# Kernel tuning notes

Hardware: AMD Instinct MI355X
Metric: run time of the kernel (lower is better)

Reference implementation:

```python
import jax, jax.numpy as jnp
import numpy as np

LEN_C = 1024
LR = 0.01
GAMMA = 0.999
R, S, E = 4, 4, 4


def setup_inputs() -> dict:
    key = jax.random.key(0)
    k1, k2, k3 = jax.random.split(key, 3)
    Fx = jax.random.normal(k1, (R, S, E, LEN_C), dtype=jnp.float32)
    Dis = jax.random.normal(k2, (E, LEN_C), dtype=jnp.float32)
    initial_weights = jax.random.normal(k3, (R, S, LEN_C), dtype=jnp.float32) * 0.02
    return {"Fx": Fx, "Dis": Dis, "initial_weights": initial_weights}


def reference(Fx, Dis, initial_weights):
    len_c = Fx.shape[-1]
    # --- first_grad: one-step adaptation gradient (detached in original torch code) ---
    w0 = jax.lax.stop_gradient(initial_weights)
    anti = jnp.einsum('rsen,rsn->e', Fx, w0)           # [E]
    error = Dis[:, -1] - anti                           # [E]
    # d/dw of sum_e error_e^2 with error = Dis - Fx.w  =>  -2 * Fx^T error
    weights_grad = jax.lax.stop_gradient(-2.0 * jnp.einsum('rsen,e->rsn', Fx, error))
    control_weights = initial_weights - 0.5 * LR * weights_grad  # [R,S,N]
    # --- build_delay_line, vectorized Toeplitz gather:
    # Fx_extend[t, r, s, e, n] = Fx[r, s, e, t-n] if t >= n else 0
    t = jnp.arange(len_c)
    idx = t[:, None] - t[None, :]                       # [T, N]
    mask = idx >= 0
    safe_idx = jnp.where(mask, idx, 0)
    Fx_ext = jnp.where(mask, Fx[..., safe_idx], jnp.float32(0.0))  # [R,S,E,T,N]
    # --- adaptive_filtering: sum over r, s, n ---
    anti_noise_matrix = jnp.einsum('rsetn,rsn->te', Fx_ext, control_weights)  # [T,E]
    gamma_vector = jnp.power(jnp.float32(GAMMA), (len_c - 1 - t).astype(jnp.float32))
    return anti_noise_matrix, gamma_vector
```

## Files before the change

### kernel.cpp

```cpp
#include <hip/hip_runtime.h>

#define LEN_C 1024
#define LR_F 0.01f
#define GAMMA_F 0.999f

__global__ __launch_bounds__(256) void k_fused(const float* __restrict__ Fx,
                                               const float* __restrict__ Dis,
                                               const float* __restrict__ w0,
                                               float* __restrict__ out) {
    int bid = blockIdx.x;
    int tid = threadIdx.x;
    int e = bid / 40;
    int r = bid % 40;
    int Tb, Nb;
    if (r < 4)       { Tb = 0; Nb = r; }
    else if (r < 12) { Tb = 1; Nb = r - 4; }
    else if (r < 24) { Tb = 2; Nb = r - 12; }
    else             { Tb = 3; Nb = r - 24; }
    const int T0 = Tb * 256, N0 = Nb * 64;
    const int B = T0 - N0 - 63;

    __shared__ __align__(16) float sFx[16 * 320];
    __shared__ __align__(16) float sCw[16 * 64];
    __shared__ float sPart[4][4];
    __shared__ float sErr[4];

    if (bid < 4) {
        int g = bid * 256 + tid;
        out[4 * LEN_C + g] = powf(GAMMA_F, (float)(LEN_C - 1 - g));
    }

    for (int rs = 0; rs < 16; ++rs) {
        const float* src = Fx + (rs * 4 + e) * LEN_C;
        for (int m = tid; m < 320; m += 256) {
            int k = B + m;
            sFx[rs * 320 + m] = ((unsigned)k < (unsigned)LEN_C) ? src[k] : 0.f;
        }
    }

    float a0 = 0.f, a1 = 0.f, a2 = 0.f, a3 = 0.f;
    #pragma unroll 4
    for (int i = tid; i < 4096; i += 256) {
        int rs = i >> 8;
        int n4 = i & 255;
        const float4* fx = (const float4*)(Fx + rs * (4 * LEN_C)) + n4;
        float4 wv = ((const float4*)(w0 + rs * LEN_C))[n4];
        float4 f0 = fx[0], f1 = fx[256], f2 = fx[512], f3 = fx[768];
        a0 += f0.x * wv.x + f0.y * wv.y + f0.z * wv.z + f0.w * wv.w;
        a1 += f1.x * wv.x + f1.y * wv.y + f1.z * wv.z + f1.w * wv.w;
        a2 += f2.x * wv.x + f2.y * wv.y + f2.z * wv.z + f2.w * wv.w;
        a3 += f3.x * wv.x + f3.y * wv.y + f3.z * wv.z + f3.w * wv.w;
    }
    for (int off = 32; off > 0; off >>= 1) {
        a0 += __shfl_down(a0, off, 64);
        a1 += __shfl_down(a1, off, 64);
        a2 += __shfl_down(a2, off, 64);
        a3 += __shfl_down(a3, off, 64);
    }
    int w = tid >> 6, l = tid & 63;
    if (l == 0) { sPart[w][0] = a0; sPart[w][1] = a1; sPart[w][2] = a2; sPart[w][3] = a3; }
    __syncthreads();
    if (tid < 4) {
        float anti = sPart[0][tid] + sPart[1][tid] + sPart[2][tid] + sPart[3][tid];
        sErr[tid] = Dis[tid * LEN_C + (LEN_C - 1)] - anti;
    }
    __syncthreads();

    {
        int rs = tid >> 4, j4 = (tid & 15) * 4;
        int n = N0 + j4;
        const float* base = Fx + rs * (4 * LEN_C) + n;
        float4 wv = *(const float4*)(w0 + rs * LEN_C + n);
        float4 f0 = *(const float4*)(base);
        float4 f1 = *(const float4*)(base + LEN_C);
        float4 f2 = *(const float4*)(base + 2 * LEN_C);
        float4 f3 = *(const float4*)(base + 3 * LEN_C);
        float e0 = sErr[0], e1 = sErr[1], e2 = sErr[2], e3 = sErr[3];
        float4 c;
        c.x = wv.x + LR_F * (f0.x * e0 + f1.x * e1 + f2.x * e2 + f3.x * e3);
        c.y = wv.y + LR_F * (f0.y * e0 + f1.y * e1 + f2.y * e2 + f3.y * e3);
        c.z = wv.z + LR_F * (f0.z * e0 + f1.z * e1 + f2.z * e2 + f3.z * e3);
        c.w = wv.w + LR_F * (f0.w * e0 + f1.w * e1 + f2.w * e2 + f3.w * e3);
        *(float4*)(sCw + rs * 64 + j4) = c;
    }
    __syncthreads();

    int i0 = l * 4;
    float acc0 = 0.f, acc1 = 0.f, acc2 = 0.f, acc3 = 0.f;
    #pragma unroll
    for (int rr = 0; rr < 4; ++rr) {
        int rs = w * 4 + rr;
        const float* crow = sCw + rs * 64;
        const float* frow = sFx + rs * 320;
        int M = i0 + 60;
        float4 flo = *(const float4*)(frow + M);
        float4 fhi = *(const float4*)(frow + M + 4);
        #pragma unroll
        for (int jb = 0; jb < 16; ++jb) {
            float4 c = *(const float4*)(crow + jb * 4);
            float v0 = flo.x, v1 = flo.y, v2 = flo.z, v3 = flo.w;
            float v4 = fhi.x, v5 = fhi.y, v6 = fhi.z;
            acc0 += v3 * c.x + v2 * c.y + v1 * c.z + v0 * c.w;
            acc1 += v4 * c.x + v3 * c.y + v2 * c.z + v1 * c.w;
            acc2 += v5 * c.x + v4 * c.y + v3 * c.z + v2 * c.w;
            acc3 += v6 * c.x + v5 * c.y + v4 * c.z + v3 * c.w;
            fhi = flo;
            M -= 4;
            if (jb < 15) flo = *(const float4*)(frow + M);
        }
    }

    __syncthreads();
    float* sred = sFx;
    sred[w * 256 + i0 + 0] = acc0;
    sred[w * 256 + i0 + 1] = acc1;
    sred[w * 256 + i0 + 2] = acc2;
    sred[w * 256 + i0 + 3] = acc3;
    __syncthreads();
    float sum = sred[tid] + sred[256 + tid] + sred[512 + tid] + sred[768 + tid];
    atomicAdd(&out[(T0 + tid) * 4 + e], sum);
}

extern "C" void kernel_launch(void* const* d_in, const int* in_sizes, int n_in,
                              void* d_out, int out_size, void* d_ws, size_t ws_size,
                              hipStream_t stream) {
    const float* Fx  = (const float*)d_in[0];
    const float* Dis = (const float*)d_in[1];
    const float* w0  = (const float*)d_in[2];
    float* out = (float*)d_out;

    hipMemsetAsync(d_out, 0, 4 * LEN_C * sizeof(float), stream);
    k_fused<<<160, 256, 0, stream>>>(Fx, Dis, w0, out);
}
```

Measured before the change: 73.66 us.

## Give each block a 32-row output tile over the full causal range, drop memset and atomics

Work is re-partitioned so each of 128 blocks owns 32 consecutive output rows for one channel and covers that row range's whole causal triangle. Each wave splits the reduction across 8 lane groups and combines them with shuffles, then writes the result directly. This removes the separate memset launch and the global atomics. In exchange the blocks are unevenly loaded, each needs about 136 KB of shared memory, and every block recomputes the full control weights for its range.

```diff
diff --git a/kernel.cpp b/kernel.cpp
--- a/kernel.cpp
+++ b/kernel.cpp
@@ -4,37 +4,38 @@
 #define LR_F 0.01f
 #define GAMMA_F 0.999f
 
-__global__ __launch_bounds__(256) void k_fused(const float* __restrict__ Fx,
-                                               const float* __restrict__ Dis,
-                                               const float* __restrict__ w0,
-                                               float* __restrict__ out) {
-    int bid = blockIdx.x;
-    int tid = threadIdx.x;
-    int e = bid / 40;
-    int r = bid % 40;
-    int Tb, Nb;
-    if (r < 4)       { Tb = 0; Nb = r; }
-    else if (r < 12) { Tb = 1; Nb = r - 4; }
-    else if (r < 24) { Tb = 2; Nb = r - 12; }
-    else             { Tb = 3; Nb = r - 24; }
-    const int T0 = Tb * 256, N0 = Nb * 64;
-    const int B = T0 - N0 - 63;
+__global__ __launch_bounds__(256) void k_one(const float* __restrict__ Fx,
+                                             const float* __restrict__ Dis,
+                                             const float* __restrict__ w0,
+                                             float* __restrict__ out) {
+    const int bid = blockIdx.x;
+    const int tid = threadIdx.x;
+    const int e  = bid >> 5;
+    const int Tb = bid & 31;
+    const int T0 = Tb << 5;
+    const int P  = T0 + 32;
+    const int S  = P >> 3;
 
-    __shared__ __align__(16) float sFx[16 * 320];
-    __shared__ __align__(16) float sCw[16 * 64];
+    __shared__ __align__(16) float sFx[16 * 1120];
+    __shared__ __align__(16) float sCw[16 * 1024];
+    __shared__ float sRed[128];
     __shared__ float sPart[4][4];
     __shared__ float sErr[4];
 
     if (bid < 4) {
-        int g = bid * 256 + tid;
+        int g = (bid << 8) + tid;
         out[4 * LEN_C + g] = powf(GAMMA_F, (float)(LEN_C - 1 - g));
     }
 
+    const int W = P + 64;
     for (int rs = 0; rs < 16; ++rs) {
         const float* src = Fx + (rs * 4 + e) * LEN_C;
-        for (int m = tid; m < 320; m += 256) {
-            int k = B + m;
-            sFx[rs * 320 + m] = ((unsigned)k < (unsigned)LEN_C) ? src[k] : 0.f;
+        float* dst = sFx + rs * 1120;
+        for (int m = tid; m < W; m += 256) {
+            int k = m - 63;
+            float v = 0.f;
+            if ((unsigned)k < (unsigned)LEN_C) v = src[k];
+            dst[m] = v;
         }
     }
 
@@ -57,7 +58,7 @@
         a2 += __shfl_down(a2, off, 64);
         a3 += __shfl_down(a3, off, 64);
     }
-    int w = tid >> 6, l = tid & 63;
+    const int w = tid >> 6, l = tid & 63;
     if (l == 0) { sPart[w][0] = a0; sPart[w][1] = a1; sPart[w][2] = a2; sPart[w][3] = a3; }
     __syncthreads();
     if (tid < 4) {
@@ -67,37 +68,42 @@
     __syncthreads();
 
     {
-        int rs = tid >> 4, j4 = (tid & 15) * 4;
-        int n = N0 + j4;
-        const float* base = Fx + rs * (4 * LEN_C) + n;
-        float4 wv = *(const float4*)(w0 + rs * LEN_C + n);
-        float4 f0 = *(const float4*)(base);
-        float4 f1 = *(const float4*)(base + LEN_C);
-        float4 f2 = *(const float4*)(base + 2 * LEN_C);
-        float4 f3 = *(const float4*)(base + 3 * LEN_C);
-        float e0 = sErr[0], e1 = sErr[1], e2 = sErr[2], e3 = sErr[3];
-        float4 c;
-        c.x = wv.x + LR_F * (f0.x * e0 + f1.x * e1 + f2.x * e2 + f3.x * e3);
-        c.y = wv.y + LR_F * (f0.y * e0 + f1.y * e1 + f2.y * e2 + f3.y * e3);
-        c.z = wv.z + LR_F * (f0.z * e0 + f1.z * e1 + f2.z * e2 + f3.z * e3);
-        c.w = wv.w + LR_F * (f0.w * e0 + f1.w * e1 + f2.w * e2 + f3.w * e3);
-        *(float4*)(sCw + rs * 64 + j4) = c;
+        int j4 = tid << 2;
+        if (j4 < P) {
+            float e0 = sErr[0], e1 = sErr[1], e2 = sErr[2], e3 = sErr[3];
+            #pragma unroll 4
+            for (int rs = 0; rs < 16; ++rs) {
+                const float* base = Fx + rs * (4 * LEN_C) + j4;
+                float4 wv = *(const float4*)(w0 + rs * LEN_C + j4);
+                float4 f0 = *(const float4*)(base);
+                float4 f1 = *(const float4*)(base + LEN_C);
+                float4 f2 = *(const float4*)(base + 2 * LEN_C);
+                float4 f3 = *(const float4*)(base + 3 * LEN_C);
+                float4 c;
+                c.x = wv.x + LR_F * (f0.x * e0 + f1.x * e1 + f2.x * e2 + f3.x * e3);
+                c.y = wv.y + LR_F * (f0.y * e0 + f1.y * e1 + f2.y * e2 + f3.y * e3);
+                c.z = wv.z + LR_F * (f0.z * e0 + f1.z * e1 + f2.z * e2 + f3.z * e3);
+                c.w = wv.w + LR_F * (f0.w * e0 + f1.w * e1 + f2.w * e2 + f3.w * e3);
+                *(float4*)(sCw + (rs << 10) + j4) = c;
+            }
+        }
     }
     __syncthreads();
 
-    int i0 = l * 4;
+    const int a = l & 7, s = l >> 3;
+    const int nb0 = s * S;
+    const int jbN = S >> 2;
     float acc0 = 0.f, acc1 = 0.f, acc2 = 0.f, acc3 = 0.f;
     #pragma unroll
     for (int rr = 0; rr < 4; ++rr) {
-        int rs = w * 4 + rr;
-        const float* crow = sCw + rs * 64;
-        const float* frow = sFx + rs * 320;
-        int M = i0 + 60;
+        int rs = (w << 2) + rr;
+        const float* frow = sFx + rs * 1120;
+        const float* crow = sCw + (rs << 10) + nb0;
+        int M = T0 + (a << 2) - nb0 + 60;
         float4 flo = *(const float4*)(frow + M);
         float4 fhi = *(const float4*)(frow + M + 4);
-        #pragma unroll
-        for (int jb = 0; jb < 16; ++jb) {
-            float4 c = *(const float4*)(crow + jb * 4);
+        for (int jb = 0; jb < jbN; ++jb) {
+            float4 c = *(const float4*)(crow + (jb << 2));
             float v0 = flo.x, v1 = flo.y, v2 = flo.z, v3 = flo.w;
             float v4 = fhi.x, v5 = fhi.y, v6 = fhi.z;
             acc0 += v3 * c.x + v2 * c.y + v1 * c.z + v0 * c.w;
@@ -106,19 +112,28 @@
             acc3 += v6 * c.x + v5 * c.y + v4 * c.z + v3 * c.w;
             fhi = flo;
             M -= 4;
-            if (jb < 15) flo = *(const float4*)(frow + M);
+            flo = *(const float4*)(frow + M);
         }
     }
 
+    for (int off = 32; off >= 8; off >>= 1) {
+        acc0 += __shfl_down(acc0, off, 64);
+        acc1 += __shfl_down(acc1, off, 64);
+        acc2 += __shfl_down(acc2, off, 64);
+        acc3 += __shfl_down(acc3, off, 64);
+    }
+    if (l < 8) {
+        int base = (w << 5) + (l << 2);
+        sRed[base + 0] = acc0;
+        sRed[base + 1] = acc1;
+        sRed[base + 2] = acc2;
+        sRed[base + 3] = acc3;
+    }
     __syncthreads();
-    float* sred = sFx;
-    sred[w * 256 + i0 + 0] = acc0;
-    sred[w * 256 + i0 + 1] = acc1;
-    sred[w * 256 + i0 + 2] = acc2;
-    sred[w * 256 + i0 + 3] = acc3;
-    __syncthreads();
-    float sum = sred[tid] + sred[256 + tid] + sred[512 + tid] + sred[768 + tid];
-    atomicAdd(&out[(T0 + tid) * 4 + e], sum);
+    if (tid < 32) {
+        float sum = sRed[tid] + sRed[32 + tid] + sRed[64 + tid] + sRed[96 + tid];
+        out[(T0 + tid) * 4 + e] = sum;
+    }
 }
 
 extern "C" void kernel_launch(void* const* d_in, const int* in_sizes, int n_in,
@@ -129,6 +144,5 @@
     const float* w0  = (const float*)d_in[2];
     float* out = (float*)d_out;
 
-    hipMemsetAsync(d_out, 0, 4 * LEN_C * sizeof(float), stream);
-    k_fused<<<160, 256, 0, stream>>>(Fx, Dis, w0, out);
+    k_one<<<128, 256, 0, stream>>>(Fx, Dis, w0, out);
 }
```

New measurement: 82.83 us. 1.12x slower.
